# Performance work log

Measured on AMD Instinct MI355X. Metric: run time of the kernel, lower is better.

## Reference

```python
import jax, jax.numpy as jnp
import numpy as np

B, H, W = 8, 56, 56
DIM = 384
NH = 8
HD = DIM // NH          # 48, also the depthwise-conv channel count
WS = 14
HID = 4 * DIM           # mlp hidden
EPS = 1e-5              # torch nn.LayerNorm default
SCALE = HD ** -0.5


def ln(x, w, b):
    m = jnp.mean(x, axis=-1, keepdims=True)
    v = jnp.var(x, axis=-1, keepdims=True)
    return (x - m) * jax.lax.rsqrt(v + EPS) * w + b


def dwconv3x3(x, w):
    # x: [N,H,W,C], w: [3,3,1,C] depthwise (groups=C), stride 1, pad 1, no bias
    return jax.lax.conv_general_dilated(
        x, w, window_strides=(1, 1), padding=((1, 1), (1, 1)),
        dimension_numbers=('NHWC', 'HWIO', 'NHWC'),
        feature_group_count=x.shape[-1])


def rel_table(rel_pos, size):
    # rel_pos: [2*size-1, HD] -> [size, size, HD] via relative coords (stride 1, q==k size)
    idx = jnp.arange(size)[:, None] - jnp.arange(size)[None, :] + (size - 1)
    return rel_pos[idx]


def win_part(x, ws):
    # [N,H,W,C] -> [N*nWh*nWw, ws, ws, C]  (H,W divisible by ws here)
    N, Hh, Ww, C = x.shape
    x = x.reshape(N, Hh // ws, ws, Ww // ws, ws, C)
    return x.transpose(0, 1, 3, 2, 4, 5).reshape(-1, ws, ws, C)


def win_unpart(x, ws, Hh, Ww):
    nW = (Hh // ws) * (Ww // ws)
    N = x.shape[0] // nW
    x = x.reshape(N, Hh // ws, Ww // ws, ws, ws, -1)
    return x.transpose(0, 1, 3, 2, 4, 5).reshape(N, Hh, Ww, -1)


def _forward(x1, x2, norm1_w, norm1_b, qkv_w, qkv_b,
             poolq_w, poolk_w, poolv_w,
             nq_w, nq_b, nk_w, nk_b, nv_w, nv_b,
             rel_h, rel_w, proj_w, proj_b,
             norm2_w, norm2_b, fc1_w, fc1_b, fc2_w, fc2_b):
    # ---- F(x1): MultiScaleAttention(norm1(x1)) ----
    xn = ln(x1, norm1_w, norm1_b)
    qkv = (xn @ qkv_w + qkv_b).reshape(B, H, W, 3, NH, HD)
    qkv = qkv.transpose(3, 0, 4, 1, 2, 5).reshape(3, B * NH, H, W, HD)
    q = ln(dwconv3x3(qkv[0], poolq_w), nq_w, nq_b)
    k = ln(dwconv3x3(qkv[1], poolk_w), nk_w, nk_b)
    v = ln(dwconv3x3(qkv[2], poolv_w), nv_w, nv_b)
    ori_q = q
    qw = win_part(q, WS).reshape(-1, WS * WS, HD)   # [Bw, 196, 48]
    kw = win_part(k, WS).reshape(-1, WS * WS, HD)
    vw = win_part(v, WS).reshape(-1, WS * WS, HD)
    attn = jnp.einsum('bqc,bkc->bqk', qw * SCALE, kw)
    # decomposed relative position bias
    Rh = rel_table(rel_h, WS)                       # [14,14,48]
    Rw = rel_table(rel_w, WS)
    rq = qw.reshape(-1, WS, WS, HD)
    bh = jnp.einsum('bhwc,hkc->bhwk', rq, Rh)
    bw = jnp.einsum('bhwc,wkc->bhwk', rq, Rw)
    attn = (attn.reshape(-1, WS, WS, WS, WS)
            + bh[:, :, :, :, None] + bw[:, :, :, None, :]).reshape(-1, WS * WS, WS * WS)
    attn = jax.nn.softmax(attn, axis=-1)
    o = jnp.einsum('bqk,bkc->bqc', attn, vw).reshape(-1, WS, WS, HD)
    o = win_unpart(o, WS, H, W)
    o = o + ori_q                                    # residual pooling
    o = o.reshape(B, NH, H, W, HD).transpose(0, 2, 3, 1, 4).reshape(B, H, W, DIM)
    f = o @ proj_w + proj_b
    y1 = x1 + f
    # ---- G(y1): Mlp(norm2(y1)) ----
    yn = ln(y1, norm2_w, norm2_b)
    g = jax.nn.gelu(yn @ fc1_w + fc1_b, approximate=False) @ fc2_w + fc2_b
    y2 = x2 + g
    return y1, y2


def setup_inputs() -> dict:
    key = jax.random.key(0)
    ks = jax.random.split(key, 32)
    p = lambda i, shape, s: jax.random.normal(ks[i], shape, jnp.float32) * s
    return {
        'x1': jax.random.normal(ks[0], (B, H, W, DIM), jnp.float32),
        'x2': jax.random.normal(ks[1], (B, H, W, DIM), jnp.float32),
        'norm1_w': jnp.ones((DIM,), jnp.float32),
        'norm1_b': jnp.zeros((DIM,), jnp.float32),
        'qkv_w': p(2, (DIM, 3 * DIM), 0.02),
        'qkv_b': jnp.zeros((3 * DIM,), jnp.float32),
        'poolq_w': p(3, (3, 3, 1, HD), 0.1),
        'poolk_w': p(4, (3, 3, 1, HD), 0.1),
        'poolv_w': p(5, (3, 3, 1, HD), 0.1),
        'nq_w': jnp.ones((HD,), jnp.float32), 'nq_b': jnp.zeros((HD,), jnp.float32),
        'nk_w': jnp.ones((HD,), jnp.float32), 'nk_b': jnp.zeros((HD,), jnp.float32),
        'nv_w': jnp.ones((HD,), jnp.float32), 'nv_b': jnp.zeros((HD,), jnp.float32),
        'rel_h': p(6, (2 * WS - 1, HD), 0.02),
        'rel_w': p(7, (2 * WS - 1, HD), 0.02),
        'proj_w': p(8, (DIM, DIM), 0.02),
        'proj_b': jnp.zeros((DIM,), jnp.float32),
        'norm2_w': jnp.ones((DIM,), jnp.float32),
        'norm2_b': jnp.zeros((DIM,), jnp.float32),
        'fc1_w': p(9, (DIM, HID), 0.02),
        'fc1_b': jnp.zeros((HID,), jnp.float32),
        'fc2_w': p(10, (HID, DIM), 0.02),
        'fc2_b': jnp.zeros((DIM,), jnp.float32),
    }


def reference(x1, x2, norm1_w, norm1_b, qkv_w, qkv_b,
              poolq_w, poolk_w, poolv_w,
              nq_w, nq_b, nk_w, nk_b, nv_w, nv_b,
              rel_h, rel_w, proj_w, proj_b,
              norm2_w, norm2_b, fc1_w, fc1_b, fc2_w, fc2_b):
    return _forward(x1, x2, norm1_w, norm1_b, qkv_w, qkv_b,
                    poolq_w, poolk_w, poolv_w,
                    nq_w, nq_b, nk_w, nk_b, nv_w, nv_b,
                    rel_h, rel_w, proj_w, proj_b,
                    norm2_w, norm2_b, fc1_w, fc1_b, fc2_w, fc2_b)
```

## Files before the change

### kernel.cpp

```cpp
#include <hip/hip_runtime.h>
#include <hip/hip_bf16.h>

typedef unsigned short u16;
typedef unsigned int u32;

#define DEVI __device__ __forceinline__

constexpr int BB = 8, HHc = 56, WWc = 56, DIMC = 384, NHC = 8, HDC = 48, WSZ = 14;
constexpr int NTOK = BB * HHc * WWc;
constexpr int HIDC = 4 * DIMC;
constexpr float EPSF = 1e-5f;
constexpr float SCALEF = 0.14433756729740643f;

typedef short bf16x8 __attribute__((ext_vector_type(8)));
typedef float f32x4 __attribute__((ext_vector_type(4)));

DEVI float b2f(u16 u) { u32 x = ((u32)u) << 16; float f; __builtin_memcpy(&f, &x, 4); return f; }
DEVI float uasf(u32 x) { float f; __builtin_memcpy(&f, &x, 4); return f; }
DEVI u16 f2b(float f) {
  u32 x; __builtin_memcpy(&x, &f, 4);
  u32 r = (x >> 16) & 1u; x += 0x7fffu + r;
  return (u16)(x >> 16);
}

DEVI float wred_sum(float v) {
  #pragma unroll
  for (int o = 32; o; o >>= 1) v += __shfl_xor(v, o);
  return v;
}

#define GLOAD_LDS16(g, l) __builtin_amdgcn_global_load_lds( \
    (const __attribute__((address_space(1))) u32*)(g), \
    (__attribute__((address_space(3))) u32*)(l), 16, 0, 0)

__global__ __launch_bounds__(256)
void wcvt_kernel(const float* __restrict__ in, u16* __restrict__ out, int K, int N) {
  __shared__ float t[32][33];
  int bk = blockIdx.x * 32, bn = blockIdx.y * 32;
  int tx = threadIdx.x & 31, ty = threadIdx.x >> 5;
  #pragma unroll
  for (int i = 0; i < 32; i += 8)
    t[ty + i][tx] = in[(size_t)(bk + ty + i) * N + bn + tx];
  __syncthreads();
  #pragma unroll
  for (int i = 0; i < 32; i += 8)
    out[(size_t)(bn + ty + i) * K + bk + tx] = f2b(t[tx][ty + i]);
}

__global__ __launch_bounds__(256)
void ln384_kernel(const float* __restrict__ x, const float* __restrict__ w,
                  const float* __restrict__ b, u16* __restrict__ out) {
  int wave = threadIdx.x >> 6, lane = threadIdx.x & 63;
  int tok = blockIdx.x * 4 + wave;
  if (tok >= NTOK) return;
  const float* xr = x + (size_t)tok * DIMC;
  float v[6]; float s = 0.f, ss = 0.f;
  #pragma unroll
  for (int i = 0; i < 6; ++i) {
    v[i] = xr[lane + i * 64];
    s += v[i]; ss += v[i] * v[i];
  }
  s = wred_sum(s); ss = wred_sum(ss);
  float mean = s * (1.f / 384.f);
  float var = ss * (1.f / 384.f) - mean * mean;
  float inv = rsqrtf(var + EPSF);
  u16* orow = out + (size_t)tok * DIMC;
  #pragma unroll
  for (int i = 0; i < 6; ++i) {
    int c = lane + i * 64;
    orow[c] = f2b((v[i] - mean) * inv * w[c] + b[c]);
  }
}

template<int MODE>
__global__ __launch_bounds__(256)
void mgemm_kernel(const u16* __restrict__ A, const u16* __restrict__ Wt,
                  const float* __restrict__ bias, const float* __restrict__ res,
                  void* __restrict__ outv, int M, int N, int K) {
  __shared__ __attribute__((aligned(16))) u16 As[2][128 * 32];
  __shared__ __attribute__((aligned(16))) u16 Bs[2][128 * 32];
  int tid = threadIdx.x;
  int wave = tid >> 6, lane = tid & 63;
  int wr = wave >> 1, wc = wave & 1;
  int bm0 = blockIdx.x * 128, bn0 = blockIdx.y * 128;
  int lrow = lane >> 2;
  int slot = (lane & 3) ^ ((lane >> 3) & 3);
  const u16* ag0 = A  + (size_t)(bm0 + wave * 32 + lrow) * K + slot * 8;
  const u16* ag1 = ag0 + (size_t)16 * K;
  const u16* bg0 = Wt + (size_t)(bn0 + wave * 32 + lrow) * K + slot * 8;
  const u16* bg1 = bg0 + (size_t)16 * K;
  int q4 = lane >> 4, r16 = lane & 15;
  int rslot = (q4 ^ ((r16 >> 1) & 3)) * 8;
  int aoff = (wr * 64 + r16) * 32 + rslot;
  int boff = (wc * 64 + r16) * 32 + rslot;
  f32x4 acc[4][4] = {};
  int nk = K >> 5;
  {
    u16* a0 = As[0] + wave * 1024;
    u16* b0 = Bs[0] + wave * 1024;
    GLOAD_LDS16(ag0, a0);
    GLOAD_LDS16(ag1, a0 + 512);
    GLOAD_LDS16(bg0, b0);
    GLOAD_LDS16(bg1, b0 + 512);
  }
  __syncthreads();
  int cur = 0;
  for (int t = 0; t < nk; ++t) {
    if (t + 1 < nk) {
      int k0 = (t + 1) << 5;
      u16* a0 = As[cur ^ 1] + wave * 1024;
      u16* b0 = Bs[cur ^ 1] + wave * 1024;
      GLOAD_LDS16(ag0 + k0, a0);
      GLOAD_LDS16(ag1 + k0, a0 + 512);
      GLOAD_LDS16(bg0 + k0, b0);
      GLOAD_LDS16(bg1 + k0, b0 + 512);
    }
    const u16* ar = As[cur] + aoff;
    const u16* br = Bs[cur] + boff;
    bf16x8 af[4], bf[4];
    #pragma unroll
    for (int f = 0; f < 4; ++f) {
      af[f] = *reinterpret_cast<const bf16x8*>(ar + f * 512);
      bf[f] = *reinterpret_cast<const bf16x8*>(br + f * 512);
    }
    #pragma unroll
    for (int fm = 0; fm < 4; ++fm)
      #pragma unroll
      for (int fn = 0; fn < 4; ++fn)
        acc[fm][fn] = __builtin_amdgcn_mfma_f32_16x16x32_bf16(af[fm], bf[fn], acc[fm][fn], 0, 0, 0);
    __syncthreads();
    cur ^= 1;
  }
  int c0 = bn0 + wc * 64 + r16;
  int r0 = bm0 + wr * 64 + q4 * 4;
  #pragma unroll
  for (int fm = 0; fm < 4; ++fm) {
    #pragma unroll
    for (int fn = 0; fn < 4; ++fn) {
      int c = c0 + fn * 16;
      float bsv = bias[c];
      #pragma unroll
      for (int j = 0; j < 4; ++j) {
        int r = r0 + fm * 16 + j;
        float v = acc[fm][fn][j] + bsv;
        if constexpr (MODE == 0) {
          u16* out = (u16*)outv;
          int s = c / DIMC; int rem = c - s * DIMC;
          int nh = rem / HDC; int ch = rem - nh * HDC;
          int b = r / 3136; int hw = r - b * 3136;
          out[(((size_t)(s * 64 + b * 8 + nh)) * 3136 + hw) * 48 + ch] = f2b(v);
        } else if constexpr (MODE == 1) {
          float* out = (float*)outv;
          size_t idx = (size_t)r * N + c;
          out[idx] = v + res[idx];
        } else {
          u16* out = (u16*)outv;
          size_t idx = (size_t)r * N + c;
          out[idx] = f2b(0.5f * v * (1.0f + erff(v * 0.70710678118654752440f)));
        }
      }
    }
  }
}

__global__ __launch_bounds__(256)
void convln_kernel(const u16* __restrict__ qkv,
                   const float* __restrict__ wq, const float* __restrict__ wk, const float* __restrict__ wv,
                   const float* __restrict__ gq, const float* __restrict__ bq,
                   const float* __restrict__ gk, const float* __restrict__ bk,
                   const float* __restrict__ gv, const float* __restrict__ bv,
                   u16* __restrict__ out) {
  __shared__ __attribute__((aligned(16))) float wsm[432];
  __shared__ __attribute__((aligned(16))) float gsm[48];
  __shared__ __attribute__((aligned(16))) float bsm[48];
  int tid = threadIdx.x;
  int sb = blockIdx.y;
  int s = sb >> 6;
  const float* wgt = (s == 0) ? wq : ((s == 1) ? wk : wv);
  const float* gam = (s == 0) ? gq : ((s == 1) ? gk : gv);
  const float* bet = (s == 0) ? bq : ((s == 1) ? bk : bv);
  for (int i = tid; i < 432; i += 256) wsm[i] = wgt[i];
  if (tid < 48) { gsm[tid] = gam[tid]; bsm[tid] = bet[tid]; }
  __syncthreads();
  int hw = blockIdx.x * 256 + tid;
  if (hw >= 3136) return;
  int h = hw / 56, w = hw - h * 56;
  const u16* img = qkv + (size_t)sb * (3136 * 48);
  float acc[48];
  #pragma unroll
  for (int c = 0; c < 48; ++c) acc[c] = 0.f;
  #pragma unroll
  for (int dy = -1; dy <= 1; ++dy) {
    int hh = h + dy;
    if ((unsigned)hh >= 56u) continue;
    #pragma unroll
    for (int dx = -1; dx <= 1; ++dx) {
      int ww = w + dx;
      if ((unsigned)ww >= 56u) continue;
      const uint4* p = reinterpret_cast<const uint4*>(img + (size_t)(hh * 56 + ww) * 48);
      const float4* wr = reinterpret_cast<const float4*>(wsm + ((dy + 1) * 3 + (dx + 1)) * 48);
      #pragma unroll
      for (int g = 0; g < 6; ++g) {
        uint4 v = p[g];
        float4 w0 = wr[g * 2], w1 = wr[g * 2 + 1];
        acc[g * 8 + 0] += uasf(v.x << 16)          * w0.x;
        acc[g * 8 + 1] += uasf(v.x & 0xFFFF0000u)  * w0.y;
        acc[g * 8 + 2] += uasf(v.y << 16)          * w0.z;
        acc[g * 8 + 3] += uasf(v.y & 0xFFFF0000u)  * w0.w;
        acc[g * 8 + 4] += uasf(v.z << 16)          * w1.x;
        acc[g * 8 + 5] += uasf(v.z & 0xFFFF0000u)  * w1.y;
        acc[g * 8 + 6] += uasf(v.w << 16)          * w1.z;
        acc[g * 8 + 7] += uasf(v.w & 0xFFFF0000u)  * w1.w;
      }
    }
  }
  float sum = 0.f, ssq = 0.f;
  #pragma unroll
  for (int c = 0; c < 48; ++c) { sum += acc[c]; ssq += acc[c] * acc[c]; }
  float mean = sum * (1.f / 48.f);
  float var = ssq * (1.f / 48.f) - mean * mean;
  float inv = rsqrtf(var + EPSF);
  u16* op = out + ((size_t)sb * 3136 + hw) * 48;
  #pragma unroll
  for (int g = 0; g < 6; ++g) {
    const float4 gm0 = *reinterpret_cast<const float4*>(gsm + g * 8);
    const float4 gm1 = *reinterpret_cast<const float4*>(gsm + g * 8 + 4);
    const float4 bt0 = *reinterpret_cast<const float4*>(bsm + g * 8);
    const float4 bt1 = *reinterpret_cast<const float4*>(bsm + g * 8 + 4);
    uint4 ov;
    u32 a0 = f2b((acc[g * 8 + 0] - mean) * inv * gm0.x + bt0.x);
    u32 a1 = f2b((acc[g * 8 + 1] - mean) * inv * gm0.y + bt0.y);
    u32 a2 = f2b((acc[g * 8 + 2] - mean) * inv * gm0.z + bt0.z);
    u32 a3 = f2b((acc[g * 8 + 3] - mean) * inv * gm0.w + bt0.w);
    u32 a4 = f2b((acc[g * 8 + 4] - mean) * inv * gm1.x + bt1.x);
    u32 a5 = f2b((acc[g * 8 + 5] - mean) * inv * gm1.y + bt1.y);
    u32 a6 = f2b((acc[g * 8 + 6] - mean) * inv * gm1.z + bt1.z);
    u32 a7 = f2b((acc[g * 8 + 7] - mean) * inv * gm1.w + bt1.w);
    ov.x = a0 | (a1 << 16);
    ov.y = a2 | (a3 << 16);
    ov.z = a4 | (a5 << 16);
    ov.w = a6 | (a7 << 16);
    *reinterpret_cast<uint4*>(op + g * 8) = ov;
  }
}

#define MFMA16(a, b, c) __builtin_amdgcn_mfma_f32_16x16x32_bf16((a), (b), (c), 0, 0, 0)
constexpr int LDP = 224;
constexpr int LDK = 104;
constexpr int LDV = 228;
__global__ __launch_bounds__(512, 1)
void attn_kernel(const u16* __restrict__ qkvc, const float* __restrict__ rel_h,
                 const float* __restrict__ rel_w, u16* __restrict__ obuf) {
  __shared__ __attribute__((aligned(16))) u16 KL[208 * LDK];
  __shared__ __attribute__((aligned(16))) u16 VT[48 * LDV];
  __shared__ __attribute__((aligned(16))) u16 QE[208 * 56];
  __shared__ __attribute__((aligned(16))) u16 PB[8 * 16 * LDP];

  int wid = blockIdx.x;
  int bnh = wid >> 4, wrem = wid & 15, wh = wrem >> 2, wwn = wrem & 3;
  int tid = threadIdx.x;
  int wave = tid >> 6, lane = tid & 63;
  int q4 = lane >> 4, r16 = lane & 15;

  { u32* z;
    z = (u32*)KL; for (int i = tid; i < 208 * LDK / 2; i += 512) z[i] = 0;
    z = (u32*)VT; for (int i = tid; i < 48 * LDV / 2; i += 512) z[i] = 0;
    z = (u32*)PB; for (int i = tid; i < 64 * 72 / 2; i += 512) z[i] = 0;
  }
  __syncthreads();
  size_t qbase = (size_t)bnh * 3136 * 48;
  size_t kbase = ((size_t)(64 + bnh) * 3136) * 48;
  size_t vbase = ((size_t)(128 + bnh) * 3136) * 48;
  for (int i = tid; i < 196 * 12; i += 512) {
    int r = i / 12, c4 = (i - r * 12) * 4;
    int h = wh * 14 + r / 14, w = wwn * 14 + r % 14;
    size_t g = (size_t)(h * 56 + w) * 48 + c4;
    ushort4 kv = *reinterpret_cast<const ushort4*>(qkvc + kbase + g);
    kv.x = f2b(b2f(kv.x) * SCALEF); kv.y = f2b(b2f(kv.y) * SCALEF);
    kv.z = f2b(b2f(kv.z) * SCALEF); kv.w = f2b(b2f(kv.w) * SCALEF);
    *reinterpret_cast<ushort4*>(KL + r * LDK + c4) = kv;
    ushort4 vv = *reinterpret_cast<const ushort4*>(qkvc + vbase + g);
    VT[(c4 + 0) * LDV + r] = vv.x; VT[(c4 + 1) * LDV + r] = vv.y;
    VT[(c4 + 2) * LDV + r] = vv.z; VT[(c4 + 3) * LDV + r] = vv.w;
  }
  for (int r = tid; r < 208; r += 512) {
    if (r < 196) {
      KL[r * LDK + 48 + r / 14] = 0x3F80;
      KL[r * LDK + 62 + r % 14] = 0x3F80;
    } else {
      KL[r * LDK + 76] = 0x3F80;
    }
  }
  for (int i = tid; i < 54 * 48; i += 512) {
    int r = i / 48, c = i - r * 48;
    float v = (r < 27) ? rel_h[r * 48 + c] : rel_w[(r - 27) * 48 + c];
    PB[r * 72 + c] = f2b(v);
  }
  __syncthreads();
  for (int mf = wave; mf < 13; mf += 8) {
    int qrow = mf * 16 + r16; int qc = qrow < 196 ? qrow : 195;
    int hq = wh * 14 + qc / 14, wq = wwn * 14 + qc % 14;
    const u16* qpg = qkvc + qbase + (size_t)(hq * 56 + wq) * 48;
    bf16x8 af0 = *reinterpret_cast<const bf16x8*>(qpg + q4 * 8);
    bf16x8 af1 = {0, 0, 0, 0, 0, 0, 0, 0};
    if (q4 < 2) af1 = *reinterpret_cast<const bf16x8*>(qpg + 32 + q4 * 8);
    #pragma unroll
    for (int nf = 0; nf < 4; ++nf) {
      bf16x8 b0 = *reinterpret_cast<const bf16x8*>(PB + (nf * 16 + r16) * 72 + q4 * 8);
      bf16x8 b1 = *reinterpret_cast<const bf16x8*>(PB + (nf * 16 + r16) * 72 + 32 + q4 * 8);
      f32x4 acc = {};
      acc = MFMA16(af0, b0, acc);
      acc = MFMA16(af1, b1, acc);
      int col = nf * 16 + r16;
      if (col < 54) {
        #pragma unroll
        for (int j = 0; j < 4; ++j)
          QE[(mf * 16 + q4 * 4 + j) * 56 + col] = f2b(acc[j]);
      }
    }
  }
  __syncthreads();
  u16 bhv[14], bwv[14];
  {
    int t = tid;
    if (t < 208) {
      int qc = t < 196 ? t : 195;
      int qh = qc / 14, qw = qc - qh * 14;
      const u16* src = QE + t * 56;
      #pragma unroll
      for (int z = 0; z < 14; ++z) {
        bhv[z] = src[qh + 13 - z];
        bwv[z] = src[27 + qw + 13 - z];
      }
    }
  }
  __syncthreads();
  {
    int t = tid;
    if (t < 208) {
      u16* dst = QE + t * 56;
      #pragma unroll
      for (int z = 0; z < 14; ++z) { dst[z] = bhv[z]; dst[14 + z] = bwv[z]; }
      dst[28] = f2b(-30000.0f);
      #pragma unroll
      for (int z = 29; z < 56; ++z) dst[z] = 0;
    }
  }
  u16* Pw = PB + wave * 16 * LDP;
  for (int i = lane; i < 16 * 16; i += 64) {
    int r = i >> 4;
    Pw[r * LDP + ((208 + (i & 15)) ^ (((r >> 2) & 3) << 3))] = 0;
  }
  __syncthreads();
  int bI = bnh >> 3, nhI = bnh & 7;
  for (int mf = wave; mf < 13; mf += 8) {
    int qrow = mf * 16 + r16; int qc = qrow < 196 ? qrow : 195;
    int hq = wh * 14 + qc / 14, wq = wwn * 14 + qc % 14;
    const u16* qpg = qkvc + qbase + (size_t)(hq * 56 + wq) * 48;
    const u16* qe = QE + qrow * 56;
    bf16x8 af0 = *reinterpret_cast<const bf16x8*>(qpg + q4 * 8);
    bf16x8 af1;
    if (q4 < 2) af1 = *reinterpret_cast<const bf16x8*>(qpg + 32 + q4 * 8);
    else        af1 = *reinterpret_cast<const bf16x8*>(qe + (q4 - 2) * 8);
    bf16x8 af2 = *reinterpret_cast<const bf16x8*>(qe + 16 + q4 * 8);
    f32x4 s[13];
    #pragma unroll
    for (int nf = 0; nf < 13; ++nf) {
      const u16* kr = KL + (nf * 16 + r16) * LDK;
      bf16x8 b0 = *reinterpret_cast<const bf16x8*>(kr + q4 * 8);
      bf16x8 b1 = *reinterpret_cast<const bf16x8*>(kr + 32 + q4 * 8);
      bf16x8 b2 = *reinterpret_cast<const bf16x8*>(kr + 64 + q4 * 8);
      f32x4 a = {};
      a = MFMA16(af0, b0, a);
      a = MFMA16(af1, b1, a);
      a = MFMA16(af2, b2, a);
      s[nf] = a;
    }
    int rowb = mf * 16 + q4 * 4;
    float mrow[4], den[4];
    #pragma unroll
    for (int j = 0; j < 4; ++j) {
      float mm = s[0][j];
      #pragma unroll
      for (int nf = 1; nf < 13; ++nf) mm = fmaxf(mm, s[nf][j]);
      #pragma unroll
      for (int off = 1; off < 16; off <<= 1) mm = fmaxf(mm, __shfl_xor(mm, off));
      mrow[j] = mm; den[j] = 0.f;
    }
    #pragma unroll
    for (int nf = 0; nf < 13; ++nf) {
      #pragma unroll
      for (int j = 0; j < 4; ++j) {
        float p = __expf(s[nf][j] - mrow[j]);
        den[j] += p;
        Pw[(q4 * 4 + j) * LDP + (((nf * 16 + r16) ^ (q4 << 3)))] = f2b(p);
      }
    }
    #pragma unroll
    for (int j = 0; j < 4; ++j)
      #pragma unroll
      for (int off = 1; off < 16; off <<= 1) den[j] += __shfl_xor(den[j], off);
    f32x4 o[3] = {};
    #pragma unroll
    for (int ks = 0; ks < 7; ++ks) {
      bf16x8 ap = *reinterpret_cast<const bf16x8*>(
          Pw + r16 * LDP + ((ks * 32 + q4 * 8) ^ (((r16 >> 2) & 3) << 3)));
      #pragma unroll
      for (int nf3 = 0; nf3 < 3; ++nf3) {
        bf16x8 bv = *reinterpret_cast<const bf16x8*>(VT + (nf3 * 16 + r16) * LDV + ks * 32 + q4 * 8);
        o[nf3] = MFMA16(ap, bv, o[nf3]);
      }
    }
    #pragma unroll
    for (int j = 0; j < 4; ++j) {
      int row = rowb + j;
      if (row < 196) {
        float rden = 1.f / den[j];
        int rh = row / 14;
        int h = wh * 14 + rh, w = wwn * 14 + row - rh * 14;
        const u16* qg = qkvc + qbase + (size_t)(h * 56 + w) * 48;
        u16* op = obuf + ((size_t)(bI * 56 + h) * 56 + w) * 384 + nhI * 48;
        #pragma unroll
        for (int nf3 = 0; nf3 < 3; ++nf3) {
          int col = nf3 * 16 + r16;
          op[col] = f2b(o[nf3][j] * rden + b2f(qg[col]));
        }
      }
    }
  }
}

extern "C" void kernel_launch(void* const* d_in, const int* in_sizes, int n_in,
                              void* d_out, int out_size, void* d_ws, size_t ws_size,
                              hipStream_t stream) {
  const float* x1      = (const float*)d_in[0];
  const float* x2      = (const float*)d_in[1];
  const float* norm1_w = (const float*)d_in[2];
  const float* norm1_b = (const float*)d_in[3];
  const float* qkv_w   = (const float*)d_in[4];
  const float* qkv_b   = (const float*)d_in[5];
  const float* poolq_w = (const float*)d_in[6];
  const float* poolk_w = (const float*)d_in[7];
  const float* poolv_w = (const float*)d_in[8];
  const float* nq_w    = (const float*)d_in[9];
  const float* nq_b    = (const float*)d_in[10];
  const float* nk_w    = (const float*)d_in[11];
  const float* nk_b    = (const float*)d_in[12];
  const float* nv_w    = (const float*)d_in[13];
  const float* nv_b    = (const float*)d_in[14];
  const float* rel_h   = (const float*)d_in[15];
  const float* rel_w   = (const float*)d_in[16];
  const float* proj_w  = (const float*)d_in[17];
  const float* proj_b  = (const float*)d_in[18];
  const float* norm2_w = (const float*)d_in[19];
  const float* norm2_b = (const float*)d_in[20];
  const float* fc1_w   = (const float*)d_in[21];
  const float* fc1_b   = (const float*)d_in[22];
  const float* fc2_w   = (const float*)d_in[23];
  const float* fc2_b   = (const float*)d_in[24];

  u16* ws      = (u16*)d_ws;
  u16* qkv     = ws;
  u16* xn      = ws + 28901376;
  u16* qkvc    = ws + 28901376;
  u16* obuf    = ws;
  u16* h1      = ws;
  u16* yn      = ws + 48168960;
  u16* qkv_wt  = ws + 38535168;
  u16* proj_wt = ws + 9633792;
  u16* fc1_wt  = ws + 38535168;
  u16* fc2_wt  = ws + 39124992;
  float* y1 = (float*)d_out;
  float* y2 = y1 + 9633792;

  wcvt_kernel<<<dim3(12, 36), 256, 0, stream>>>(qkv_w, qkv_wt, 384, 1152);
  ln384_kernel<<<NTOK / 4, 256, 0, stream>>>(x1, norm1_w, norm1_b, xn);
  mgemm_kernel<0><<<dim3(196, 9), 256, 0, stream>>>(xn, qkv_wt, qkv_b, nullptr, qkv, NTOK, 1152, 384);
  convln_kernel<<<dim3(13, 192), 256, 0, stream>>>(qkv, poolq_w, poolk_w, poolv_w,
                                                   nq_w, nq_b, nk_w, nk_b, nv_w, nv_b, qkvc);
  wcvt_kernel<<<dim3(12, 12), 256, 0, stream>>>(proj_w, proj_wt, 384, 384);
  attn_kernel<<<1024, 512, 0, stream>>>(qkvc, rel_h, rel_w, obuf);
  wcvt_kernel<<<dim3(12, 48), 256, 0, stream>>>(fc1_w, fc1_wt, 384, 1536);
  wcvt_kernel<<<dim3(48, 12), 256, 0, stream>>>(fc2_w, fc2_wt, 1536, 384);
  mgemm_kernel<1><<<dim3(196, 3), 256, 0, stream>>>(obuf, proj_wt, proj_b, x1, y1, NTOK, 384, 384);
  ln384_kernel<<<NTOK / 4, 256, 0, stream>>>(y1, norm2_w, norm2_b, yn);
  mgemm_kernel<2><<<dim3(196, 12), 256, 0, stream>>>(yn, fc1_wt, fc1_b, nullptr, h1, NTOK, 1536, 384);
  mgemm_kernel<1><<<dim3(196, 3), 256, 0, stream>>>(h1, fc2_wt, fc2_b, x2, y2, NTOK, 384, 1536);
}
```

Measured before the change: 374.7 us.

## Triple-buffer GEMM LDS tiles with two-deep async prefetch and explicit vmcnt waits

The bf16 MFMA GEMM's shared-memory staging goes from double to triple buffering, prefetching two K-tiles ahead with direct global-to-LDS loads. __syncthreads is replaced by explicit s_waitcnt vmcnt counts and raw s_barrier, so the next tile's loads stay in flight while the current tile is computed. This aims to hide more global memory latency. In exchange it uses 50% more LDS per block, which may lower occupancy, and it relies on hand-tuned waitcnt counts being correct.

```diff
diff --git a/kernel.cpp b/kernel.cpp
--- a/kernel.cpp
+++ b/kernel.cpp
@@ -77,8 +77,8 @@
 void mgemm_kernel(const u16* __restrict__ A, const u16* __restrict__ Wt,
                   const float* __restrict__ bias, const float* __restrict__ res,
                   void* __restrict__ outv, int M, int N, int K) {
-  __shared__ __attribute__((aligned(16))) u16 As[2][128 * 32];
-  __shared__ __attribute__((aligned(16))) u16 Bs[2][128 * 32];
+  __shared__ __attribute__((aligned(16))) u16 As[3][128 * 32];
+  __shared__ __attribute__((aligned(16))) u16 Bs[3][128 * 32];
   int tid = threadIdx.x;
   int wave = tid >> 6, lane = tid & 63;
   int wr = wave >> 1, wc = wave & 1;
@@ -96,25 +96,27 @@
   f32x4 acc[4][4] = {};
   int nk = K >> 5;
   {
-    u16* a0 = As[0] + wave * 1024;
-    u16* b0 = Bs[0] + wave * 1024;
-    GLOAD_LDS16(ag0, a0);
-    GLOAD_LDS16(ag1, a0 + 512);
-    GLOAD_LDS16(bg0, b0);
-    GLOAD_LDS16(bg1, b0 + 512);
-  }
-  __syncthreads();
-  int cur = 0;
+    u16* a0 = As[0] + wave * 1024; u16* b0 = Bs[0] + wave * 1024;
+    GLOAD_LDS16(ag0, a0);       GLOAD_LDS16(ag1, a0 + 512);
+    GLOAD_LDS16(bg0, b0);       GLOAD_LDS16(bg1, b0 + 512);
+    u16* a1 = As[1] + wave * 1024; u16* b1 = Bs[1] + wave * 1024;
+    GLOAD_LDS16(ag0 + 32, a1);  GLOAD_LDS16(ag1 + 32, a1 + 512);
+    GLOAD_LDS16(bg0 + 32, b1);  GLOAD_LDS16(bg1 + 32, b1 + 512);
+  }
+  int cur = 0, pf = 2;
   for (int t = 0; t < nk; ++t) {
-    if (t + 1 < nk) {
-      int k0 = (t + 1) << 5;
-      u16* a0 = As[cur ^ 1] + wave * 1024;
-      u16* b0 = Bs[cur ^ 1] + wave * 1024;
-      GLOAD_LDS16(ag0 + k0, a0);
-      GLOAD_LDS16(ag1 + k0, a0 + 512);
-      GLOAD_LDS16(bg0 + k0, b0);
-      GLOAD_LDS16(bg1 + k0, b0 + 512);
-    }
+    if (t + 2 < nk) {
+      int k0 = (t + 2) << 5;
+      u16* a0 = As[pf] + wave * 1024; u16* b0 = Bs[pf] + wave * 1024;
+      GLOAD_LDS16(ag0 + k0, a0);  GLOAD_LDS16(ag1 + k0, a0 + 512);
+      GLOAD_LDS16(bg0 + k0, b0);  GLOAD_LDS16(bg1 + k0, b0 + 512);
+      asm volatile("s_waitcnt vmcnt(8)" ::: "memory");
+    } else if (t + 1 < nk) {
+      asm volatile("s_waitcnt vmcnt(4)" ::: "memory");
+    } else {
+      asm volatile("s_waitcnt vmcnt(0)" ::: "memory");
+    }
+    __builtin_amdgcn_s_barrier();
     const u16* ar = As[cur] + aoff;
     const u16* br = Bs[cur] + boff;
     bf16x8 af[4], bf[4];
@@ -128,8 +130,10 @@
       #pragma unroll
       for (int fn = 0; fn < 4; ++fn)
         acc[fm][fn] = __builtin_amdgcn_mfma_f32_16x16x32_bf16(af[fm], bf[fn], acc[fm][fn], 0, 0, 0);
-    __syncthreads();
-    cur ^= 1;
+    asm volatile("s_waitcnt lgkmcnt(0)" ::: "memory");
+    __builtin_amdgcn_s_barrier();
+    cur = (cur == 2) ? 0 : cur + 1;
+    pf  = (pf  == 2) ? 0 : pf  + 1;
   }
   int c0 = bn0 + wc * 64 + r16;
   int r0 = bm0 + wr * 64 + q4 * 4;
```

New measurement: 380.5 us. About the same (+1.5%).
